# Performance work log

Hardware: AMD Instinct MI355X
Metric: run time of the kernel (lower is better)

## Reference

```python
import jax, jax.numpy as jnp
from jax import lax
import numpy as np

EPS = 1e-5
K = 3


def _conv(x, w, b, pad, dil=1, groups=1):
    out = lax.conv_general_dilated(
        x, w, (1, 1), [(pad, pad), (pad, pad)], rhs_dilation=(dil, dil),
        dimension_numbers=('NCHW', 'OIHW', 'NCHW'), feature_group_count=groups)
    return out + b[None, :, None, None]


def _bn(x, g, b, m, v):
    scale = g / jnp.sqrt(v + EPS)
    return (x - m[None, :, None, None]) * scale[None, :, None, None] + b[None, :, None, None]


def setup_inputs() -> dict:
    key = jax.random.key(0)
    ks = jax.random.split(key, 24)
    B, C, H, W = 8, 256, 48, 80
    Hd = 256  # hidden_channels
    n = lambda k, s, sc=0.05: (jax.random.normal(k, s, dtype=jnp.float32) * sc)
    return {
        'f_t_minus_2': jax.random.normal(ks[0], (B, C, H, W), dtype=jnp.float32),
        'f_t_minus_1': jax.random.normal(ks[1], (B, C, H, W), dtype=jnp.float32),
        'f_t':         jax.random.normal(ks[2], (B, C, H, W), dtype=jnp.float32),
        'ov_w1': n(ks[3], (Hd, 3 * C, 3, 3)), 'ov_b1': n(ks[4], (Hd,)),
        'bn1_g': jnp.ones((Hd,), jnp.float32), 'bn1_b': jnp.zeros((Hd,), jnp.float32),
        'bn1_m': n(ks[5], (Hd,)), 'bn1_v': jax.random.uniform(ks[6], (Hd,), jnp.float32, 0.5, 1.5),
        'ov_w2': n(ks[7], (Hd, Hd, 3, 3)), 'ov_b2': n(ks[8], (Hd,)),
        'bn2_g': jnp.ones((Hd,), jnp.float32), 'bn2_b': jnp.zeros((Hd,), jnp.float32),
        'bn2_m': n(ks[9], (Hd,)), 'bn2_v': jax.random.uniform(ks[10], (Hd,), jnp.float32, 0.5, 1.5),
        'g_w': n(ks[11], (C, Hd, 1, 1)), 'g_b': n(ks[12], (C,)),
        'fc1_w': n(ks[13], (512, 2 * C)), 'fc1_b': n(ks[14], (512,)),
        'fc2_w': n(ks[15], (C * K * K, 512)), 'fc2_b': n(ks[16], (C * K * K,)),
        'ap_w': n(ks[17], (1, 2 * C, 1, 1)), 'ap_b': n(ks[18], (1,)),
        'a_w': n(ks[19], (1, 2 * C, 1, 1)), 'a_b': jnp.ones((1,), jnp.float32),
    }


def reference(f_t_minus_2, f_t_minus_1, f_t,
              ov_w1, ov_b1, bn1_g, bn1_b, bn1_m, bn1_v,
              ov_w2, ov_b2, bn2_g, bn2_b, bn2_m, bn2_v,
              g_w, g_b, fc1_w, fc1_b, fc2_w, fc2_b,
              ap_w, ap_b, a_w, a_b):
    B, C, H, W = f_t.shape
    # (1) Overview-Net (GCM)
    f_concat = jnp.concatenate([f_t_minus_2, f_t_minus_1, f_t], axis=1)
    h = jax.nn.relu(_bn(_conv(f_concat, ov_w1, ov_b1, pad=2, dil=2), bn1_g, bn1_b, bn1_m, bn1_v))
    h = jax.nn.relu(_bn(_conv(h, ov_w2, ov_b2, pad=4, dil=4), bn2_g, bn2_b, bn2_m, bn2_v))
    g_pooled = h.mean(axis=(2, 3), keepdims=True)            # [B,Hd,1,1]
    G = _conv(g_pooled, g_w, g_b, pad=0)                     # [B,C,1,1]
    # (2) Focus-Net: FC-generated per-(batch,channel) 3x3 depthwise conv on (f_t, f_{t-1})
    Fs = jnp.concatenate([f_t, f_t_minus_1], axis=0)         # [2B,C,H,W]
    g_flat = jnp.repeat(G.reshape(B, C), 2, axis=0)          # [2B,C]
    gap = Fs.mean(axis=(2, 3))                               # [2B,C]
    fc_in = jnp.concatenate([g_flat, gap], axis=1)           # [2B,2C]
    w = jax.nn.silu(fc_in @ fc1_w.T + fc1_b) @ fc2_w.T + fc2_b  # [2B, C*9]
    w = w.reshape(2 * B * C, 1, K, K)
    x = Fs.reshape(1, 2 * B * C, H, W)
    out = lax.conv_general_dilated(
        x, w, (1, 1), [(1, 1), (1, 1)],
        dimension_numbers=('NCHW', 'OIHW', 'NCHW'), feature_group_count=2 * B * C)
    out = out.reshape(2 * B, C, H, W)
    f_t_mod, f_t1_mod = out[:B], out[B:]
    # (3) Dynamic fusion
    f_prev_cat = jnp.concatenate([f_t1_mod, f_t_minus_2], axis=1)
    alpha_prev = 0.3 + 0.4 * jax.nn.sigmoid(_conv(f_prev_cat, ap_w, ap_b, pad=0))
    f_prev = alpha_prev * f_t1_mod + (1.0 - alpha_prev) * f_t_minus_2
    f_cat = jnp.concatenate([f_t_mod, f_prev], axis=1)
    alpha = 0.6 + 0.3 * jax.nn.sigmoid(_conv(f_cat, a_w, a_b, pad=0))
    return alpha * f_t_mod + (1.0 - alpha) * f_prev
```

## Files before the change

### kernel.cpp

```cpp
#include <hip/hip_runtime.h>
#include <hip/hip_bf16.h>
#include <math.h>


typedef __bf16 bf16x8 __attribute__((ext_vector_type(8)));
typedef float f32x4 __attribute__((ext_vector_type(4)));
typedef __attribute__((address_space(1))) void as1_void;
typedef __attribute__((address_space(3))) void as3_void;


__global__ __launch_bounds__(256) void prep_consts_kernel(
    const float* __restrict__ ob1, const float* __restrict__ g1, const float* __restrict__ b1,
    const float* __restrict__ m1, const float* __restrict__ v1,
    const float* __restrict__ ob2, const float* __restrict__ g2, const float* __restrict__ b2,
    const float* __restrict__ m2, const float* __restrict__ v2,
    float* __restrict__ cst)
{
  int i = threadIdx.x;
  float a1 = g1[i] / sqrtf(v1[i] + 1e-5f);
  cst[i]       = a1;
  cst[256 + i] = (ob1[i] - m1[i]) * a1 + b1[i];
  float a2 = g2[i] / sqrtf(v2[i] + 1e-5f);
  cst[512 + i] = a2;
  cst[768 + i] = (ob2[i] - m2[i]) * a2 + b2[i];
}

__global__ __launch_bounds__(256) void pad_concat_kernel(
    const float* __restrict__ f2, const float* __restrict__ f1, const float* __restrict__ f0,
    __hip_bfloat16* __restrict__ out)
{
  int bid = blockIdx.x;
  const int cg = bid % 6; bid /= 6;
  const int y = bid % 48;
  const int b = bid / 48;

  __shared__ float tile[128 * 85];

  const float* src = (cg < 2) ? f2 : ((cg < 4) ? f1 : f0);
  const int ccbase = (cg & 1) * 128;

#pragma unroll
  for (int it = 0; it < 10; it++) {
    const int idx = it * 256 + threadIdx.x;
    const int cl = idx / 20, x4 = idx % 20;
    const float4 v = *(const float4*)(src +
        (((size_t)b * 256 + ccbase + cl) * 48 + y) * 80 + x4 * 4);
    float* t = tile + cl * 85 + x4 * 4;
    t[0] = v.x; t[1] = v.y; t[2] = v.z; t[3] = v.w;
  }
  __syncthreads();

  __hip_bfloat16* obase = out + ((size_t)(b * 52 + y + 2) * 84 + 2) * 768 + cg * 128;
#pragma unroll
  for (int it = 0; it < 5; it++) {
    const int idx = it * 256 + threadIdx.x;
    const int chunk = idx & 15, x = idx >> 4;
    const float* t = tile + chunk * 8 * 85 + x;
    union { __hip_bfloat16 h[8]; uint4 u; } pk;
#pragma unroll
    for (int j = 0; j < 8; j++) pk.h[j] = __float2bfloat16(t[j * 85]);
    *(uint4*)(obase + (size_t)x * 768 + chunk * 8) = pk.u;
  }
}

__global__ __launch_bounds__(256) void repack_w_kernel(
    const float* __restrict__ w, __hip_bfloat16* __restrict__ out, int OC, int IC)
{
  int idx = blockIdx.x * 256 + threadIdx.x;
  if (idx >= OC * IC * 9) return;
  int ic = idx % IC;
  int t = idx / IC;
  int oc = t % OC;
  int tap = t / OC;
  out[idx] = __float2bfloat16(w[(oc * IC + ic) * 9 + tap]);
}

__global__ __launch_bounds__(256) void gap_kernel(
    const float* __restrict__ f0, const float* __restrict__ f1, float* __restrict__ gapv)
{
  int i = blockIdx.x >> 8, c = blockIdx.x & 255;
  const float* src = (i < 8) ? (f0 + ((size_t)i * 256 + c) * 3840)
                             : (f1 + ((size_t)(i - 8) * 256 + c) * 3840);
  float s = 0.f;
  for (int k = threadIdx.x; k < 3840; k += 256) s += src[k];
  for (int off = 32; off; off >>= 1) s += __shfl_xor(s, off);
  __shared__ float red[4];
  if ((threadIdx.x & 63) == 0) red[threadIdx.x >> 6] = s;
  __syncthreads();
  if (threadIdx.x == 0)
    gapv[blockIdx.x] = (red[0] + red[1] + red[2] + red[3]) * (1.f / 3840.f);
}

template <int CIN, int HP, int WP, int DIL, int MODE>
__global__ __launch_bounds__(256) void conv_mfma_kernel(
    const __hip_bfloat16* __restrict__ inp, const __hip_bfloat16* __restrict__ wt,
    const float* __restrict__ bnA, const float* __restrict__ bnB,
    __hip_bfloat16* __restrict__ outp, float* __restrict__ gpool)
{
  __shared__ unsigned short As[8192] __attribute__((aligned(16)));
  __shared__ unsigned short Bs[8192] __attribute__((aligned(16)));

  int bid = blockIdx.x;
  bid = (bid & 7) * 60 + (bid >> 3);
  const int ocb = bid & 1; bid >>= 1;
  const int xb = bid % 5; bid /= 5;
  const int yb = bid % 6; bid /= 6;
  const int b = bid;
  const int y0 = yb * 8, x0 = xb * 16, oc0 = ocb * 128;

  const int t = threadIdx.x;
  const int w = t >> 6, l = t & 63;
  const int col16 = l & 15, quad = l >> 4;
  const int wm = w >> 1, wn = w & 1;
  const int rsub = l >> 3;
  const int jj = (l & 7) ^ rsub;

  f32x4 acc[4][4];
  const f32x4 zf = {0.f, 0.f, 0.f, 0.f};
#pragma unroll
  for (int i = 0; i < 4; i++)
#pragma unroll
    for (int j = 0; j < 4; j++) acc[i][j] = zf;

  for (int c0 = 0; c0 < CIN; c0 += 64) {
    for (int tap = 0; tap < 9; tap++) {
      const int ty = tap / 3, tx = tap - ty * 3;
      const __hip_bfloat16* inBase =
          inp + ((size_t)(b * HP + y0 + DIL * ty) * WP + (x0 + DIL * tx)) * CIN + jj * 8 + c0;
      const __hip_bfloat16* wBase = wt + (size_t)(tap * 256 + oc0) * CIN + jj * 8 + c0;
      __syncthreads();
#pragma unroll
      for (int i = 0; i < 4; i++) {
        const int q = i * 4 + w;
        const int m = q * 8 + rsub;
        const int ry = m >> 4, rx = m & 15;
        const __hip_bfloat16* gp = inBase + (ry * WP + rx) * CIN;
        __builtin_amdgcn_global_load_lds((as1_void*)gp,
            (as3_void*)((char*)As + q * 1024), 16, 0, 0);
      }
#pragma unroll
      for (int i = 0; i < 4; i++) {
        const int q = i * 4 + w;
        const int n = q * 8 + rsub;
        const __hip_bfloat16* gp = wBase + n * CIN;
        __builtin_amdgcn_global_load_lds((as1_void*)gp,
            (as3_void*)((char*)Bs + q * 1024), 16, 0, 0);
      }
      __syncthreads();
#pragma unroll
      for (int kiter = 0; kiter < 2; kiter++) {
        bf16x8 af[4], bg[4];
#pragma unroll
        for (int fi = 0; fi < 4; fi++) {
          const int m = wm * 64 + fi * 16 + col16;
          const int jc = (kiter * 4 + quad) ^ (m & 7);
          af[fi] = *(const bf16x8*)((const char*)As + m * 128 + jc * 16);
        }
#pragma unroll
        for (int fi = 0; fi < 4; fi++) {
          const int n = wn * 64 + fi * 16 + col16;
          const int jc = (kiter * 4 + quad) ^ (n & 7);
          bg[fi] = *(const bf16x8*)((const char*)Bs + n * 128 + jc * 16);
        }
#pragma unroll
        for (int fm_ = 0; fm_ < 4; fm_++)
#pragma unroll
          for (int fn_ = 0; fn_ < 4; fn_++)
            acc[fm_][fn_] = __builtin_amdgcn_mfma_f32_16x16x32_bf16(
                af[fm_], bg[fn_], acc[fm_][fn_], 0, 0, 0);
      }
    }
  }

  if (MODE == 0) {
#pragma unroll
    for (int fn_ = 0; fn_ < 4; fn_++) {
      const int oc = oc0 + wn * 64 + fn_ * 16 + col16;
      const float sa = bnA[oc], sb = bnB[oc];
#pragma unroll
      for (int fm_ = 0; fm_ < 4; fm_++) {
#pragma unroll
        for (int r = 0; r < 4; r++) {
          const int m = wm * 64 + fm_ * 16 + quad * 4 + r;
          const int y = y0 + (m >> 4), x = x0 + (m & 15);
          const float v = fmaxf(acc[fm_][fn_][r] * sa + sb, 0.f);
          outp[((size_t)(b * 56 + y + 4) * 88 + (x + 4)) * 256 + oc] = __float2bfloat16(v);
        }
      }
    }
  } else {
#pragma unroll
    for (int fn_ = 0; fn_ < 4; fn_++) {
      const int oc = oc0 + wn * 64 + fn_ * 16 + col16;
      const float sa = bnA[oc], sb = bnB[oc];
      float cs = 0.f;
#pragma unroll
      for (int fm_ = 0; fm_ < 4; fm_++)
#pragma unroll
        for (int r = 0; r < 4; r++)
          cs += fmaxf(acc[fm_][fn_][r] * sa + sb, 0.f);
      cs += __shfl_xor(cs, 16);
      cs += __shfl_xor(cs, 32);
      if (quad == 0) atomicAdd(&gpool[b * 256 + oc], cs);
    }
  }
}


__global__ __launch_bounds__(256) void fcG_kernel(
    const float* __restrict__ gpool, const float* __restrict__ gw,
    const float* __restrict__ gb, float* __restrict__ G)
{
  int b = blockIdx.x, oc = threadIdx.x;
  __shared__ float pool[256];
  pool[oc] = gpool[b * 256 + oc] * (1.f / 3840.f);
  __syncthreads();
  float s = gb[oc];
  const float* wr = gw + oc * 256;
  for (int c2 = 0; c2 < 256; c2++) s += pool[c2] * wr[c2];
  G[b * 256 + oc] = s;
}

__global__ __launch_bounds__(256) void fc1_kernel(
    const float* __restrict__ G, const float* __restrict__ gapv,
    const float* __restrict__ w, const float* __restrict__ bias,
    float* __restrict__ out1)
{
  __shared__ float fin[16][513];
  for (int idx = threadIdx.x; idx < 16 * 512; idx += 256) {
    int i = idx >> 9, k = idx & 511;
    fin[i][k] = (k < 256) ? G[(i >> 1) * 256 + k] : gapv[i * 256 + (k - 256)];
  }
  __syncthreads();
  int g = blockIdx.x * 256 + threadIdx.x;
  int j = g >> 4, i = g & 15;
  float s = bias[j];
  const float* wr = w + j * 512;
  for (int k = 0; k < 512; k++) s += fin[i][k] * wr[k];
  out1[j * 16 + i] = s / (1.f + expf(-s));
}

__global__ __launch_bounds__(256) void fc2_kernel(
    const float* __restrict__ out1, const float* __restrict__ w,
    const float* __restrict__ bias, float* __restrict__ wdw)
{
  __shared__ float fin[16][513];
  for (int idx = threadIdx.x; idx < 16 * 512; idx += 256) {
    int i = idx >> 9, k = idx & 511;
    fin[i][k] = out1[k * 16 + i];
  }
  __syncthreads();
  int g = blockIdx.x * 256 + threadIdx.x;
  int j = g >> 4, i = g & 15;
  float s = bias[j];
  const float* wr = w + j * 512;
  for (int k = 0; k < 512; k++) s += fin[i][k] * wr[k];
  wdw[i * 2304 + j] = s;
}

__global__ __launch_bounds__(256) void dw_kernel(
    const float* __restrict__ f0, const float* __restrict__ f1,
    const float* __restrict__ wdw, float* __restrict__ fm)
{
  int i = blockIdx.x >> 8, c = blockIdx.x & 255;
  const float* src = (i < 8) ? (f0 + ((size_t)i * 256 + c) * 3840)
                             : (f1 + ((size_t)(i - 8) * 256 + c) * 3840);
  float* dst = fm + ((size_t)i * 256 + c) * 3840;
  __shared__ float w9[9];
  if (threadIdx.x < 9) w9[threadIdx.x] = wdw[i * 2304 + c * 9 + threadIdx.x];
  __syncthreads();
  for (int p = threadIdx.x; p < 3840; p += 256) {
    int y = p / 80, x = p - y * 80;
    float s = 0.f;
#pragma unroll
    for (int ky = 0; ky < 3; ky++) {
      int yy = y + ky - 1;
      if (yy < 0 || yy >= 48) continue;
#pragma unroll
      for (int kx = 0; kx < 3; kx++) {
        int xx = x + kx - 1;
        if (xx < 0 || xx >= 80) continue;
        s += w9[ky * 3 + kx] * src[yy * 80 + xx];
      }
    }
    dst[p] = s;
  }
}

__global__ __launch_bounds__(320) void alpha_kernel(
    const float* __restrict__ fm, const float* __restrict__ f2,
    const float* __restrict__ apw, const float* __restrict__ apb,
    const float* __restrict__ aw, const float* __restrict__ ab,
    float* __restrict__ planes)
{
  int b = blockIdx.x / 48, y = blockIdx.x % 48;
  int x = threadIdx.x % 80, g = threadIdx.x / 80;
  const float* ftm  = fm + ((size_t)b * 256) * 3840 + y * 80 + x;
  const float* ft1m = fm + ((size_t)(b + 8) * 256) * 3840 + y * 80 + x;
  const float* ptm2 = f2 + ((size_t)b * 256) * 3840 + y * 80 + x;
  float S = 0.f, T0 = 0.f, T1 = 0.f, T2 = 0.f;
  for (int cc = 0; cc < 64; cc++) {
    int c = g * 64 + cc;
    float v1 = ft1m[(size_t)c * 3840];
    float v2 = ptm2[(size_t)c * 3840];
    float v0 = ftm[(size_t)c * 3840];
    S  += apw[c] * v1 + apw[256 + c] * v2;
    T0 += aw[c] * v0;
    T1 += aw[256 + c] * v1;
    T2 += aw[256 + c] * v2;
  }
  __shared__ float red[4][4][80];
  red[0][g][x] = S; red[1][g][x] = T0; red[2][g][x] = T1; red[3][g][x] = T2;
  __syncthreads();
  if (g == 0) {
    S  = red[0][0][x] + red[0][1][x] + red[0][2][x] + red[0][3][x];
    T0 = red[1][0][x] + red[1][1][x] + red[1][2][x] + red[1][3][x];
    T1 = red[2][0][x] + red[2][1][x] + red[2][2][x] + red[2][3][x];
    T2 = red[3][0][x] + red[3][1][x] + red[3][2][x] + red[3][3][x];
    float ap = 0.3f + 0.4f / (1.f + expf(-(S + apb[0])));
    float A  = T0 + ap * T1 + (1.f - ap) * T2 + ab[0];
    float al = 0.6f + 0.3f / (1.f + expf(-A));
    planes[blockIdx.x * 80 + x]         = ap;
    planes[30720 + blockIdx.x * 80 + x] = al;
  }
}

__global__ __launch_bounds__(256) void final_kernel(
    const float* __restrict__ fm, const float* __restrict__ f2,
    const float* __restrict__ planes, float* __restrict__ out)
{
  size_t idx = ((size_t)blockIdx.x * 256 + threadIdx.x) * 4;
  if (idx >= (size_t)7864320) return;
  int bc = (int)(idx / 3840);
  int p  = (int)(idx % 3840);
  int b  = bc >> 8;
  int pix = b * 3840 + p;
  const float4 vm = *(const float4*)(fm + (size_t)bc * 3840 + p);
  const float4 v1 = *(const float4*)(fm + ((size_t)bc + 2048) * 3840 + p);
  const float4 v2 = *(const float4*)(f2 + (size_t)bc * 3840 + p);
  const float4 ap = *(const float4*)(planes + pix);
  const float4 al = *(const float4*)(planes + 30720 + pix);
  float4 r;
  r.x = al.x * vm.x + (1.f - al.x) * (ap.x * v1.x + (1.f - ap.x) * v2.x);
  r.y = al.y * vm.y + (1.f - al.y) * (ap.y * v1.y + (1.f - ap.y) * v2.y);
  r.z = al.z * vm.z + (1.f - al.z) * (ap.z * v1.z + (1.f - ap.z) * v2.z);
  r.w = al.w * vm.w + (1.f - al.w) * (ap.w * v1.w + (1.f - ap.w) * v2.w);
  *(float4*)(out + idx) = r;
}


extern "C" void kernel_launch(void* const* d_in, const int* in_sizes, int n_in,
                              void* d_out, int out_size, void* d_ws, size_t ws_size,
                              hipStream_t stream)
{
  const float* f_tm2 = (const float*)d_in[0];
  const float* f_tm1 = (const float*)d_in[1];
  const float* f_t   = (const float*)d_in[2];
  const float* ov_w1 = (const float*)d_in[3];
  const float* ov_b1 = (const float*)d_in[4];
  const float* bn1_g = (const float*)d_in[5];
  const float* bn1_b = (const float*)d_in[6];
  const float* bn1_m = (const float*)d_in[7];
  const float* bn1_v = (const float*)d_in[8];
  const float* ov_w2 = (const float*)d_in[9];
  const float* ov_b2 = (const float*)d_in[10];
  const float* bn2_g = (const float*)d_in[11];
  const float* bn2_b = (const float*)d_in[12];
  const float* bn2_m = (const float*)d_in[13];
  const float* bn2_v = (const float*)d_in[14];
  const float* g_w   = (const float*)d_in[15];
  const float* g_b   = (const float*)d_in[16];
  const float* fc1_w = (const float*)d_in[17];
  const float* fc1_b = (const float*)d_in[18];
  const float* fc2_w = (const float*)d_in[19];
  const float* fc2_b = (const float*)d_in[20];
  const float* ap_w  = (const float*)d_in[21];
  const float* ap_b  = (const float*)d_in[22];
  const float* a_w   = (const float*)d_in[23];
  const float* a_b   = (const float*)d_in[24];

  char* ws = (char*)d_ws;
  float* fm            = (float*)ws;
  __hip_bfloat16* in1p = (__hip_bfloat16*)ws;
  __hip_bfloat16* wt1  = (__hip_bfloat16*)(ws + 53673984);
  __hip_bfloat16* wt2  = (__hip_bfloat16*)(ws + 57212928);
  __hip_bfloat16* h1p  = (__hip_bfloat16*)(ws + 58392576);
  float* gpool         = (float*)(ws + 78577664);
  float* gapv          = (float*)(ws + 78585856);
  float* Gv            = (float*)(ws + 78602240);
  float* out1          = (float*)(ws + 78610432);
  float* wdw           = (float*)(ws + 78643200);
  float* planes        = (float*)(ws + 78790656);
  float* cst           = (float*)(ws + 79036416);

  hipMemsetAsync(in1p, 0, 53673984, stream);
  hipMemsetAsync(h1p, 0, 20185088, stream);
  hipMemsetAsync(gpool, 0, 8192, stream);

  prep_consts_kernel<<<1, 256, 0, stream>>>(ov_b1, bn1_g, bn1_b, bn1_m, bn1_v,
                                            ov_b2, bn2_g, bn2_b, bn2_m, bn2_v, cst);
  pad_concat_kernel<<<2304, 256, 0, stream>>>(f_tm2, f_tm1, f_t, in1p);
  repack_w_kernel<<<6912, 256, 0, stream>>>(ov_w1, wt1, 256, 768);
  repack_w_kernel<<<2304, 256, 0, stream>>>(ov_w2, wt2, 256, 256);
  gap_kernel<<<4096, 256, 0, stream>>>(f_t, f_tm1, gapv);

  conv_mfma_kernel<768, 52, 84, 2, 0><<<480, 256, 0, stream>>>(in1p, wt1, cst, cst + 256, h1p, nullptr);
  conv_mfma_kernel<256, 56, 88, 4, 1><<<480, 256, 0, stream>>>(h1p, wt2, cst + 512, cst + 768, nullptr, gpool);

  fcG_kernel<<<8, 256, 0, stream>>>(gpool, g_w, g_b, Gv);
  fc1_kernel<<<32, 256, 0, stream>>>(Gv, gapv, fc1_w, fc1_b, out1);
  fc2_kernel<<<144, 256, 0, stream>>>(out1, fc2_w, fc2_b, wdw);
  dw_kernel<<<4096, 256, 0, stream>>>(f_t, f_tm1, wdw, fm);
  alpha_kernel<<<384, 320, 0, stream>>>(fm, f_tm2, ap_w, ap_b, a_w, a_b, planes);
  final_kernel<<<7680, 256, 0, stream>>>(fm, f_tm2, planes, (float*)d_out);
}
```

Measured before the change: 526.1 us.

## Double-buffer LDS tiles in MFMA conv to overlap loads with compute

```diff
diff --git a/kernel.cpp b/kernel.cpp
--- a/kernel.cpp
+++ b/kernel.cpp
@@ -97,8 +97,8 @@
     const float* __restrict__ bnA, const float* __restrict__ bnB,
     __hip_bfloat16* __restrict__ outp, float* __restrict__ gpool)
 {
-  __shared__ unsigned short As[8192] __attribute__((aligned(16)));
-  __shared__ unsigned short Bs[8192] __attribute__((aligned(16)));
+  __shared__ unsigned short As[2][8192] __attribute__((aligned(16)));
+  __shared__ unsigned short Bs[2][8192] __attribute__((aligned(16)));
 
   int bid = blockIdx.x;
   bid = (bid & 7) * 60 + (bid >> 3);
@@ -122,54 +122,64 @@
 #pragma unroll
     for (int j = 0; j < 4; j++) acc[i][j] = zf;
 
-  for (int c0 = 0; c0 < CIN; c0 += 64) {
-    for (int tap = 0; tap < 9; tap++) {
-      const int ty = tap / 3, tx = tap - ty * 3;
-      const __hip_bfloat16* inBase =
-          inp + ((size_t)(b * HP + y0 + DIL * ty) * WP + (x0 + DIL * tx)) * CIN + jj * 8 + c0;
-      const __hip_bfloat16* wBase = wt + (size_t)(tap * 256 + oc0) * CIN + jj * 8 + c0;
-      __syncthreads();
-#pragma unroll
-      for (int i = 0; i < 4; i++) {
-        const int q = i * 4 + w;
-        const int m = q * 8 + rsub;
-        const int ry = m >> 4, rx = m & 15;
-        const __hip_bfloat16* gp = inBase + (ry * WP + rx) * CIN;
-        __builtin_amdgcn_global_load_lds((as1_void*)gp,
-            (as3_void*)((char*)As + q * 1024), 16, 0, 0);
+  constexpr int NS = (CIN / 64) * 9;
+
+  auto stage = [&](int s, int sel) {
+    const int ci = s / 9;
+    const int tap = s - ci * 9;
+    const int c0 = ci * 64;
+    const int ty = tap / 3, tx = tap - ty * 3;
+    const __hip_bfloat16* inBase =
+        inp + ((size_t)(b * HP + y0 + DIL * ty) * WP + (x0 + DIL * tx)) * CIN + jj * 8 + c0;
+    const __hip_bfloat16* wBase = wt + (size_t)(tap * 256 + oc0) * CIN + jj * 8 + c0;
+#pragma unroll
+    for (int i = 0; i < 4; i++) {
+      const int q = i * 4 + w;
+      const int m = q * 8 + rsub;
+      const int ry = m >> 4, rx = m & 15;
+      __builtin_amdgcn_global_load_lds((as1_void*)(inBase + (ry * WP + rx) * CIN),
+          (as3_void*)((char*)As[sel] + q * 1024), 16, 0, 0);
+    }
+#pragma unroll
+    for (int i = 0; i < 4; i++) {
+      const int q = i * 4 + w;
+      const int n = q * 8 + rsub;
+      __builtin_amdgcn_global_load_lds((as1_void*)(wBase + n * CIN),
+          (as3_void*)((char*)Bs[sel] + q * 1024), 16, 0, 0);
+    }
+  };
+
+  stage(0, 0);
+  int cur = 0;
+  for (int s = 0; s < NS; ++s) {
+    __syncthreads();
+    if (s + 1 < NS) stage(s + 1, cur ^ 1);
+
+    const char* Ab = (const char*)As[cur];
+    const char* Bb = (const char*)Bs[cur];
+#pragma unroll
+    for (int kiter = 0; kiter < 2; kiter++) {
+      bf16x8 af[4], bg[4];
+#pragma unroll
+      for (int fi = 0; fi < 4; fi++) {
+        const int m = wm * 64 + fi * 16 + col16;
+        const int jc = (kiter * 4 + quad) ^ (m & 7);
+        af[fi] = *(const bf16x8*)(Ab + m * 128 + jc * 16);
       }
 #pragma unroll
-      for (int i = 0; i < 4; i++) {
-        const int q = i * 4 + w;
-        const int n = q * 8 + rsub;
-        const __hip_bfloat16* gp = wBase + n * CIN;
-        __builtin_amdgcn_global_load_lds((as1_void*)gp,
-            (as3_void*)((char*)Bs + q * 1024), 16, 0, 0);
+      for (int fi = 0; fi < 4; fi++) {
+        const int n = wn * 64 + fi * 16 + col16;
+        const int jc = (kiter * 4 + quad) ^ (n & 7);
+        bg[fi] = *(const bf16x8*)(Bb + n * 128 + jc * 16);
       }
-      __syncthreads();
-#pragma unroll
-      for (int kiter = 0; kiter < 2; kiter++) {
-        bf16x8 af[4], bg[4];
-#pragma unroll
-        for (int fi = 0; fi < 4; fi++) {
-          const int m = wm * 64 + fi * 16 + col16;
-          const int jc = (kiter * 4 + quad) ^ (m & 7);
-          af[fi] = *(const bf16x8*)((const char*)As + m * 128 + jc * 16);
-        }
-#pragma unroll
-        for (int fi = 0; fi < 4; fi++) {
-          const int n = wn * 64 + fi * 16 + col16;
-          const int jc = (kiter * 4 + quad) ^ (n & 7);
-          bg[fi] = *(const bf16x8*)((const char*)Bs + n * 128 + jc * 16);
-        }
-#pragma unroll
-        for (int fm_ = 0; fm_ < 4; fm_++)
-#pragma unroll
-          for (int fn_ = 0; fn_ < 4; fn_++)
-            acc[fm_][fn_] = __builtin_amdgcn_mfma_f32_16x16x32_bf16(
-                af[fm_], bg[fn_], acc[fm_][fn_], 0, 0, 0);
-      }
-    }
+#pragma unroll
+      for (int fm_ = 0; fm_ < 4; fm_++)
+#pragma unroll
+        for (int fn_ = 0; fn_ < 4; fn_++)
+          acc[fm_][fn_] = __builtin_amdgcn_mfma_f32_16x16x32_bf16(
+              af[fm_], bg[fn_], acc[fm_][fn_], 0, 0, 0);
+    }
+    cur ^= 1;
   }
 
   if (MODE == 0) {
```

New measurement: 580.1 us. 10.3% more time.
